# Optimization experiments

Hardware: AMD Instinct MI355X
Metric: run time of the kernel (lower is better)

The kernel has to match this reference:

```python
import jax, jax.numpy as jnp
import numpy as np

NUM_CLASSES = 80
NUM_ANCHORS = 5
ANCHORS = np.array([[1.3221, 1.73145], [3.19275, 4.00944], [5.05587, 8.09892],
                    [9.47112, 4.84053], [11.2364, 10.0071]], dtype=np.float32)
OBJECT_SCALE = 5.0
NOOBJECT_SCALE = 1.0
COORD_SCALE = 1.0
CLASS_SCALE = 1.0
THRESH = 0.6
SEEN = 0  # module initializes self.seen = 0 -> burn-in branch (seen < 12800) active
MAX_BOXES = 50


def _iou_cxcywh(a, b):
    # a, b: (..., 4) center-x, center-y, w, h; broadcastable. Matches multi_bbox_ious(x1y1x2y2=False).
    ax1, ax2 = a[..., 0] - a[..., 2] / 2, a[..., 0] + a[..., 2] / 2
    ay1, ay2 = a[..., 1] - a[..., 3] / 2, a[..., 1] + a[..., 3] / 2
    bx1, bx2 = b[..., 0] - b[..., 2] / 2, b[..., 0] + b[..., 2] / 2
    by1, by2 = b[..., 1] - b[..., 3] / 2, b[..., 1] + b[..., 3] / 2
    iw = jnp.maximum(jnp.minimum(ax2, bx2) - jnp.maximum(ax1, bx1), 0.0)
    ih = jnp.maximum(jnp.minimum(ay2, by2) - jnp.maximum(ay1, by1), 0.0)
    inter = iw * ih
    union = a[..., 2] * a[..., 3] + b[..., 2] * b[..., 3] - inter
    return inter / jnp.maximum(union, 1e-10)


def setup_inputs() -> dict:
    key = jax.random.key(0)
    k1, k2, k3, k4, k5, k6 = jax.random.split(key, 6)
    nB, nH, nW = 64, 38, 38
    output = jax.random.normal(k1, (nB, NUM_ANCHORS * (5 + NUM_CLASSES), nH, nW), dtype=jnp.float32)
    # target rows: (class, x, y, w, h), coords normalized to (0,1); x>0 keeps all 50 boxes valid
    cls = jax.random.randint(k2, (nB, MAX_BOXES), 0, NUM_CLASSES).astype(jnp.float32)
    x = jax.random.uniform(k3, (nB, MAX_BOXES), minval=0.05, maxval=0.95)
    y = jax.random.uniform(k4, (nB, MAX_BOXES), minval=0.05, maxval=0.95)
    w = jax.random.uniform(k5, (nB, MAX_BOXES), minval=0.02, maxval=0.4)
    h = jax.random.uniform(k6, (nB, MAX_BOXES), minval=0.02, maxval=0.4)
    target = jnp.stack([cls, x, y, w, h], axis=-1).reshape(nB, MAX_BOXES * 5)
    return {"output": output, "target": target}


def _forward(output, target):
    nB, nA, nC = output.shape[0], NUM_ANCHORS, NUM_CLASSES
    nH, nW = output.shape[2], output.shape[3]
    N = nB * nA * nH * nW
    anchors = jnp.asarray(ANCHORS)
    f32 = output.dtype

    out5 = output.reshape(nB, nA, 5 + nC, nH, nW)
    txy = jax.nn.sigmoid(out5[:, :, 0:2])  # [nB,nA,2,nH,nW]
    twh = out5[:, :, 2:4]
    conf = jax.nn.sigmoid(out5[:, :, 4]).reshape(N)
    cls_logits = out5[:, :, 5:].transpose(0, 1, 3, 4, 2).reshape(N, nC)
    # coord layout matches torch: [4, nB*nA*nH*nW], rows = (sx, sy, tw, th)
    coord = jnp.concatenate([txy, twh], axis=2).transpose(2, 0, 1, 3, 4).reshape(4, N)

    # decoded pred boxes in grid units; detached like the original (convert2cpu + .detach())
    grid_x = jnp.arange(nW, dtype=f32)
    grid_y = jnp.arange(nH, dtype=f32)[:, None]
    px = txy[:, :, 0] + grid_x
    py = txy[:, :, 1] + grid_y
    pw = jnp.exp(twh[:, :, 0]) * anchors[:, 0][None, :, None, None]
    ph = jnp.exp(twh[:, :, 1]) * anchors[:, 1][None, :, None, None]
    pred_boxes = jax.lax.stop_gradient(jnp.stack([px, py, pw, ph], axis=-1))  # [nB,nA,nH,nW,4]

    # ---------------- build_targets, vectorized over (batch, gt-box) ----------------
    tbox = target.reshape(nB, MAX_BOXES, 5)  # (cls, x, y, w, h)
    # loop breaks at first x == 0 -> prefix-valid mask
    valid = jnp.cumprod((tbox[:, :, 1] > 0).astype(jnp.int32), axis=1).astype(bool)
    gx, gy = tbox[:, :, 1] * nW, tbox[:, :, 2] * nH
    gw, gh = tbox[:, :, 3] * nW, tbox[:, :, 4] * nH
    gt = jnp.stack([gx, gy, gw, gh], axis=-1)  # [nB,50,4]

    # pass 1: ignore mask -- max IoU of every pred box against all valid GTs
    pb_flat = pred_boxes.reshape(nB, nA * nH * nW, 4)
    ious = _iou_cxcywh(pb_flat[:, :, None, :], gt[:, None, :, :])  # [nB,P,50]
    cur_ious = jnp.where(valid[:, None, :], ious, 0.0).max(axis=2)
    noobj = (cur_ious <= THRESH).astype(f32).reshape(N)

    # pass 2: best anchor per GT (both boxes centered at origin -> IoU simplifies)
    aw, ah = anchors[:, 0], anchors[:, 1]
    inter_a = jnp.minimum(aw, gw[..., None]) * jnp.minimum(ah, gh[..., None])  # [nB,50,nA]
    union_a = aw * ah + (gw * gh)[..., None] - inter_a
    best_n = jnp.argmax(inter_a / jnp.maximum(union_a, 1e-10), axis=-1)  # [nB,50]

    gi = jnp.clip(gx.astype(jnp.int32), 0, nW - 1)
    gj = jnp.clip(gy.astype(jnp.int32), 0, nH - 1)
    b_idx = jnp.arange(nB)[:, None]
    pred_sel = pred_boxes[b_idx, best_n, gj, gi]  # [nB,50,4]
    iou_sel = _iou_cxcywh(gt, pred_sel)           # [nB,50]

    fidx = ((b_idx * nA + best_n) * nH + gj) * nW + gi
    fidx = jnp.where(valid, fidx, N)  # invalid boxes -> OOB index, dropped by scatter

    obj = jnp.zeros(N, f32).at[fidx].set(1.0, mode='drop')
    noobj = noobj.at[fidx].set(0.0, mode='drop')
    cm0 = 0.01 if SEEN < 12800 else 0.0
    coord_mask = jnp.full(N, cm0, f32).at[fidx].set(2.0 - tbox[:, :, 3] * tbox[:, :, 4], mode='drop')
    t0 = 0.5 if SEEN < 12800 else 0.0
    tc0 = jnp.full(N, t0, f32).at[fidx].set(gx - gi.astype(f32), mode='drop')
    tc1 = jnp.full(N, t0, f32).at[fidx].set(gy - gj.astype(f32), mode='drop')
    tc2 = jnp.zeros(N, f32).at[fidx].set(jnp.log(gw / aw[best_n]), mode='drop')
    tc3 = jnp.zeros(N, f32).at[fidx].set(jnp.log(gh / ah[best_n]), mode='drop')
    tcoord = jnp.stack([tc0, tc1, tc2, tc3], axis=0)  # [4,N]
    tconf = jnp.zeros(N, f32).at[fidx].set(iou_sel, mode='drop')  # rescore=1
    tcls = jnp.zeros(N, jnp.int32).at[fidx].set(tbox[:, :, 0].astype(jnp.int32), mode='drop')

    # ---------------- losses ----------------
    conf_mask = OBJECT_SCALE * obj + NOOBJECT_SCALE * noobj
    loss_coord = COORD_SCALE * jnp.sum(((coord - tcoord) * coord_mask) ** 2) / nB
    loss_conf = jnp.sum(((conf - tconf) * conf_mask) ** 2) / nB
    logp = jax.nn.log_softmax(cls_logits, axis=-1)
    ce = -jnp.take_along_axis(logp, tcls[:, None], axis=1)[:, 0]  # per-cell CE
    loss_cls = CLASS_SCALE * jnp.sum(obj * ce) / nB  # CE summed only over obj cells
    return loss_coord + loss_conf + loss_cls


def reference(output, target):
    return _forward(output, target)
```

## Files before the change

### kernel.cpp

```cpp
#include <hip/hip_runtime.h>
#include <math.h>

#define NB 64
#define NA 5
#define NC 80
#define NH 38
#define NW 38
#define MAXB 50
#define PLANE (NH*NW)
#define PER_B (NA*PLANE)
#define NCH (5+NC)
#define MAIN_BX ((PER_B + 255) / 256)
#define NPART (MAIN_BX * NB)

__constant__ float c_aw[5] = {1.3221f, 3.19275f, 5.05587f, 9.47112f, 11.2364f};
__constant__ float c_ah[5] = {1.73145f, 4.00944f, 8.09892f, 4.84053f, 10.0071f};

struct Entry {
    int   fidx;
    int   tcls;
    float cm, tc0, tc1, tc2, tc3, tconf;
};

__device__ inline float sigmoidf(float x) { return 1.f / (1.f + expf(-x)); }

__device__ inline float iou_f(float ax, float ay, float aw_, float ah_,
                              float bx, float by, float bw_, float bh_) {
    float ax1 = ax - aw_ * 0.5f, ax2 = ax + aw_ * 0.5f;
    float ay1 = ay - ah_ * 0.5f, ay2 = ay + ah_ * 0.5f;
    float bx1 = bx - bw_ * 0.5f, bx2 = bx + bw_ * 0.5f;
    float by1 = by - bh_ * 0.5f, by2 = by + bh_ * 0.5f;
    float iw = fmaxf(fminf(ax2, bx2) - fmaxf(ax1, bx1), 0.f);
    float ih = fmaxf(fminf(ay2, by2) - fmaxf(ay1, by1), 0.f);
    float inter = iw * ih;
    float uni = aw_ * ah_ + bw_ * bh_ - inter;
    return inter / fmaxf(uni, 1e-10f);
}

__global__ __launch_bounds__(64)
void prep_kernel(const float* __restrict__ out, const float* __restrict__ target,
                 float4* __restrict__ gt, int* __restrict__ nvalid,
                 Entry* __restrict__ entries) {
    int b = blockIdx.x;
    int t = threadIdx.x;
    const float* tb = target + b * MAXB * 5;

    float cls = 0.f, x = 0.f, y = 0.f, w = 0.f, h = 0.f;
    bool has = (t < MAXB);
    if (has) {
        cls = tb[t * 5 + 0];
        x   = tb[t * 5 + 1];
        y   = tb[t * 5 + 2];
        w   = tb[t * 5 + 3];
        h   = tb[t * 5 + 4];
    }
    unsigned long long mask = __ballot(has && (x > 0.f));
    bool valid = has && (((~mask) & ((1ull << (t + 1)) - 1ull)) == 0ull);

    float gx = x * NW, gy = y * NH, gw = w * NW, gh = h * NH;

    int best = 0; float bestr = -1.f;
    #pragma unroll
    for (int a = 0; a < NA; a++) {
        float inter = fminf(c_aw[a], gw) * fminf(c_ah[a], gh);
        float uni   = c_aw[a] * c_ah[a] + gw * gh - inter;
        float r = inter / fmaxf(uni, 1e-10f);
        if (r > bestr) { bestr = r; best = a; }
    }
    int gi = min(max((int)gx, 0), NW - 1);
    int gj = min(max((int)gy, 0), NH - 1);
    int fidx = b * PER_B + best * PLANE + gj * NW + gi;

    float iou_sel = 0.f;
    if (valid) {
        int base = ((b * NA + best) * NCH) * PLANE + gj * NW + gi;
        float o0 = out[base];
        float o1 = out[base + PLANE];
        float o2 = out[base + 2 * PLANE];
        float o3 = out[base + 3 * PLANE];
        float px = sigmoidf(o0) + (float)gi;
        float py = sigmoidf(o1) + (float)gj;
        float pw = expf(o2) * c_aw[best];
        float ph = expf(o3) * c_ah[best];
        iou_sel = iou_f(gx, gy, gw, gh, px, py, pw, ph);
    }

    __shared__ int sfidx[64];
    sfidx[t] = valid ? fidx : -1;
    __syncthreads();
    bool winner = valid;
    if (valid) {
        for (int s = t + 1; s < MAXB; s++) {
            if (sfidx[s] == fidx) { winner = false; break; }
        }
    }

    if (has) {
        gt[b * MAXB + t] = make_float4(gx, gy, gw, gh);
        Entry e;
        e.fidx  = winner ? fidx : -1;
        e.tcls  = (int)cls;
        e.cm    = 2.f - w * h;
        e.tc0   = gx - (float)gi;
        e.tc1   = gy - (float)gj;
        e.tc2   = logf(gw / c_aw[best]);
        e.tc3   = logf(gh / c_ah[best]);
        e.tconf = iou_sel;
        entries[b * MAXB + t] = e;
    }
    if (t == 0) {
        unsigned long long nm = ~mask;
        int cnt = __ffsll((unsigned long long)nm) - 1;
        nvalid[b] = min(cnt, MAXB);
    }
}

__global__ __launch_bounds__(256)
void main_kernel(const float* __restrict__ out,
                 const float4* __restrict__ gt, const int* __restrict__ nvalid,
                 const Entry* __restrict__ entries, float* __restrict__ partial) {
    int b   = blockIdx.y;
    int tid = threadIdx.x;
    int m   = blockIdx.x * blockDim.x + tid;

    __shared__ float4 sgt[MAXB];
    __shared__ Entry  sent[MAXB];
    __shared__ int    snv;
    if (tid < MAXB) {
        sgt[tid]  = gt[b * MAXB + tid];
        sent[tid] = entries[b * MAXB + tid];
    }
    if (tid == 0) snv = nvalid[b];
    __syncthreads();

    float part = 0.f;
    if (m < PER_B) {
        int a   = m / PLANE;
        int pos = m - a * PLANE;
        int j   = pos / NW;
        int i   = pos - j * NW;

        int base = ((b * NA + a) * NCH) * PLANE + pos;
        float o0 = out[base];
        float o1 = out[base + PLANE];
        float o2 = out[base + 2 * PLANE];
        float o3 = out[base + 3 * PLANE];
        float o4 = out[base + 4 * PLANE];

        float s0   = sigmoidf(o0);
        float s1   = sigmoidf(o1);
        float conf = sigmoidf(o4);
        float px = s0 + (float)i;
        float py = s1 + (float)j;
        float pw = expf(o2) * c_aw[a];
        float ph = expf(o3) * c_ah[a];

        float curmax = 0.f;
        int nv = snv;
        for (int s = 0; s < nv; s++) {
            float4 g = sgt[s];
            curmax = fmaxf(curmax, iou_f(px, py, pw, ph, g.x, g.y, g.z, g.w));
        }

        float cm = 0.01f, tc0 = 0.5f, tc1 = 0.5f, tc2 = 0.f, tc3 = 0.f, tconf = 0.f;
        bool is_obj = false;
        int tcls = 0;
        int n = b * PER_B + m;
        for (int s = 0; s < MAXB; s++) {
            if (sent[s].fidx == n) {
                is_obj = true;
                cm  = sent[s].cm;
                tc0 = sent[s].tc0;  tc1 = sent[s].tc1;
                tc2 = sent[s].tc2;  tc3 = sent[s].tc3;
                tconf = sent[s].tconf;
                tcls  = sent[s].tcls;
            }
        }
        float conf_mask = is_obj ? 5.f : ((curmax <= 0.6f) ? 1.f : 0.f);

        float d;
        d = (s0   - tc0)   * cm;        part += d * d;
        d = (s1   - tc1)   * cm;        part += d * d;
        d = (o2   - tc2)   * cm;        part += d * d;
        d = (o3   - tc3)   * cm;        part += d * d;
        d = (conf - tconf) * conf_mask; part += d * d;

        if (is_obj) {
            const float* cp = out + base + 5 * PLANE;
            float mx = -INFINITY, s = 0.f, tv = 0.f;
            for (int c = 0; c < NC; c++) {
                float v = cp[c * PLANE];
                if (c == tcls) tv = v;
                float mn = fmaxf(mx, v);
                s = s * expf(mx - mn) + expf(v - mn);
                mx = mn;
            }
            part += mx + logf(s) - tv;
        }
    }

    for (int off = 32; off > 0; off >>= 1) part += __shfl_down(part, off);
    __shared__ float wsum[4];
    int wid = tid >> 6, lane = tid & 63;
    if (lane == 0) wsum[wid] = part;
    __syncthreads();
    if (tid == 0)
        partial[b * gridDim.x + blockIdx.x] = wsum[0] + wsum[1] + wsum[2] + wsum[3];
}

__global__ __launch_bounds__(256)
void final_kernel(const float* __restrict__ partial, float* __restrict__ loss) {
    int tid = threadIdx.x;
    float s = 0.f;
    for (int i = tid; i < NPART; i += 256) s += partial[i];
    for (int off = 32; off > 0; off >>= 1) s += __shfl_down(s, off);
    __shared__ float wsum[4];
    int wid = tid >> 6, lane = tid & 63;
    if (lane == 0) wsum[wid] = s;
    __syncthreads();
    if (tid == 0)
        loss[0] = (wsum[0] + wsum[1] + wsum[2] + wsum[3]) * (1.0f / NB);
}

extern "C" void kernel_launch(void* const* d_in, const int* in_sizes, int n_in,
                              void* d_out, int out_size, void* d_ws, size_t ws_size,
                              hipStream_t stream) {
    const float* out    = (const float*)d_in[0];
    const float* target = (const float*)d_in[1];
    float* loss = (float*)d_out;

    char* ws = (char*)d_ws;
    float4* gt      = (float4*)ws;
    int*    nvalid  = (int*)(ws + 51200);
    Entry*  entries = (Entry*)(ws + 51456);
    float*  partial = (float*)(ws + 153856);

    prep_kernel<<<NB, 64, 0, stream>>>(out, target, gt, nvalid, entries);

    dim3 grid(MAIN_BX, NB);
    main_kernel<<<grid, 256, 0, stream>>>(out, gt, nvalid, entries, partial);

    final_kernel<<<1, 256, 0, stream>>>(partial, loss);
}
```

Before: 253.5 us.

## Fuse target prep into main loss kernel and precompute GT box corners

```diff
diff --git a/kernel.cpp b/kernel.cpp
--- a/kernel.cpp
+++ b/kernel.cpp
@@ -24,115 +24,109 @@
 
 __device__ inline float sigmoidf(float x) { return 1.f / (1.f + expf(-x)); }
 
-__device__ inline float iou_f(float ax, float ay, float aw_, float ah_,
-                              float bx, float by, float bw_, float bh_) {
-    float ax1 = ax - aw_ * 0.5f, ax2 = ax + aw_ * 0.5f;
-    float ay1 = ay - ah_ * 0.5f, ay2 = ay + ah_ * 0.5f;
-    float bx1 = bx - bw_ * 0.5f, bx2 = bx + bw_ * 0.5f;
-    float by1 = by - bh_ * 0.5f, by2 = by + bh_ * 0.5f;
-    float iw = fmaxf(fminf(ax2, bx2) - fmaxf(ax1, bx1), 0.f);
-    float ih = fmaxf(fminf(ay2, by2) - fmaxf(ay1, by1), 0.f);
-    float inter = iw * ih;
-    float uni = aw_ * ah_ + bw_ * bh_ - inter;
-    return inter / fmaxf(uni, 1e-10f);
-}
-
-__global__ __launch_bounds__(64)
-void prep_kernel(const float* __restrict__ out, const float* __restrict__ target,
-                 float4* __restrict__ gt, int* __restrict__ nvalid,
-                 Entry* __restrict__ entries) {
-    int b = blockIdx.x;
-    int t = threadIdx.x;
-    const float* tb = target + b * MAXB * 5;
-
-    float cls = 0.f, x = 0.f, y = 0.f, w = 0.f, h = 0.f;
-    bool has = (t < MAXB);
-    if (has) {
-        cls = tb[t * 5 + 0];
-        x   = tb[t * 5 + 1];
-        y   = tb[t * 5 + 2];
-        w   = tb[t * 5 + 3];
-        h   = tb[t * 5 + 4];
+__global__ __launch_bounds__(256)
+void main_kernel(const float* __restrict__ out, const float* __restrict__ target,
+                 float* __restrict__ partial) {
+    const int b   = blockIdx.y;
+    const int bx  = blockIdx.x;
+    const int tid = threadIdx.x;
+
+    __shared__ float4 sbox[MAXB];
+    __shared__ float  sarea[MAXB];
+    __shared__ Entry  sent[MAXB];
+    __shared__ int    sfx[64];
+    __shared__ int    snv;
+    __shared__ int    sobj_cnt;
+    __shared__ int    sobj_idx[MAXB];
+
+    if (tid == 0) sobj_cnt = 0;
+
+    if (tid < 64) {
+        const float* tb = target + b * MAXB * 5;
+        int t = tid;
+        bool has = (t < MAXB);
+        float cls = 0.f, x = 0.f, y = 0.f, w = 0.f, h = 0.f;
+        if (has) {
+            cls = tb[t * 5 + 0];
+            x   = tb[t * 5 + 1];
+            y   = tb[t * 5 + 2];
+            w   = tb[t * 5 + 3];
+            h   = tb[t * 5 + 4];
+        }
+        unsigned long long mask = __ballot(has && (x > 0.f));
+        bool valid = has && (((~mask) & ((1ull << (t + 1)) - 1ull)) == 0ull);
+
+        float gx = x * NW, gy = y * NH, gw = w * NW, gh = h * NH;
+
+        int best = 0; float bestr = -1.f;
+        #pragma unroll
+        for (int a = 0; a < NA; a++) {
+            float inter = fminf(c_aw[a], gw) * fminf(c_ah[a], gh);
+            float uni   = c_aw[a] * c_ah[a] + gw * gh - inter;
+            float r = inter / fmaxf(uni, 1e-10f);
+            if (r > bestr) { bestr = r; best = a; }
+        }
+        int gi = min(max((int)gx, 0), NW - 1);
+        int gj = min(max((int)gy, 0), NH - 1);
+        int fidx = b * PER_B + best * PLANE + gj * NW + gi;
+
+        float iou_sel = 0.f;
+        if (valid) {
+            int base = ((b * NA + best) * NCH) * PLANE + gj * NW + gi;
+            float o0 = out[base];
+            float o1 = out[base + PLANE];
+            float o2 = out[base + 2 * PLANE];
+            float o3 = out[base + 3 * PLANE];
+            float px = sigmoidf(o0) + (float)gi;
+            float py = sigmoidf(o1) + (float)gj;
+            float pw = expf(o2) * c_aw[best];
+            float ph = expf(o3) * c_ah[best];
+            float iw = fmaxf(fminf(gx + gw*0.5f, px + pw*0.5f) - fmaxf(gx - gw*0.5f, px - pw*0.5f), 0.f);
+            float ih = fmaxf(fminf(gy + gh*0.5f, py + ph*0.5f) - fmaxf(gy - gh*0.5f, py - ph*0.5f), 0.f);
+            float inter = iw * ih;
+            float uni = gw * gh + pw * ph - inter;
+            iou_sel = inter / fmaxf(uni, 1e-10f);
+        }
+
+        sfx[t] = valid ? fidx : -1;
+        bool winner = valid;
+        if (valid) {
+            for (int s = t + 1; s < MAXB; s++)
+                if (sfx[s] == fidx) { winner = false; break; }
+        }
+
+        if (has) {
+            sbox[t]  = make_float4(gx - gw*0.5f, gy - gh*0.5f, gx + gw*0.5f, gy + gh*0.5f);
+            sarea[t] = gw * gh;
+            Entry e;
+            e.fidx  = winner ? fidx : -1;
+            e.tcls  = (int)cls;
+            e.cm    = 2.f - w * h;
+            e.tc0   = gx - (float)gi;
+            e.tc1   = gy - (float)gj;
+            e.tc2   = logf(gw / c_aw[best]);
+            e.tc3   = logf(gh / c_ah[best]);
+            e.tconf = iou_sel;
+            sent[t] = e;
+        }
+        if (t == 0) {
+            unsigned long long nm = ~mask;
+            snv = min(__ffsll((unsigned long long)nm) - 1, MAXB);
+        }
     }
-    unsigned long long mask = __ballot(has && (x > 0.f));
-    bool valid = has && (((~mask) & ((1ull << (t + 1)) - 1ull)) == 0ull);
-
-    float gx = x * NW, gy = y * NH, gw = w * NW, gh = h * NH;
-
-    int best = 0; float bestr = -1.f;
-    #pragma unroll
-    for (int a = 0; a < NA; a++) {
-        float inter = fminf(c_aw[a], gw) * fminf(c_ah[a], gh);
-        float uni   = c_aw[a] * c_ah[a] + gw * gh - inter;
-        float r = inter / fmaxf(uni, 1e-10f);
-        if (r > bestr) { bestr = r; best = a; }
+    __syncthreads();
+
+    const int nlo = b * PER_B + bx * 256;
+    if (tid < MAXB) {
+        int f = sent[tid].fidx;
+        if (f >= nlo && f < nlo + 256) {
+            int slot = atomicAdd(&sobj_cnt, 1);
+            sobj_idx[slot] = tid;
+        }
     }
-    int gi = min(max((int)gx, 0), NW - 1);
-    int gj = min(max((int)gy, 0), NH - 1);
-    int fidx = b * PER_B + best * PLANE + gj * NW + gi;
-
-    float iou_sel = 0.f;
-    if (valid) {
-        int base = ((b * NA + best) * NCH) * PLANE + gj * NW + gi;
-        float o0 = out[base];
-        float o1 = out[base + PLANE];
-        float o2 = out[base + 2 * PLANE];
-        float o3 = out[base + 3 * PLANE];
-        float px = sigmoidf(o0) + (float)gi;
-        float py = sigmoidf(o1) + (float)gj;
-        float pw = expf(o2) * c_aw[best];
-        float ph = expf(o3) * c_ah[best];
-        iou_sel = iou_f(gx, gy, gw, gh, px, py, pw, ph);
-    }
-
-    __shared__ int sfidx[64];
-    sfidx[t] = valid ? fidx : -1;
-    __syncthreads();
-    bool winner = valid;
-    if (valid) {
-        for (int s = t + 1; s < MAXB; s++) {
-            if (sfidx[s] == fidx) { winner = false; break; }
-        }
-    }
-
-    if (has) {
-        gt[b * MAXB + t] = make_float4(gx, gy, gw, gh);
-        Entry e;
-        e.fidx  = winner ? fidx : -1;
-        e.tcls  = (int)cls;
-        e.cm    = 2.f - w * h;
-        e.tc0   = gx - (float)gi;
-        e.tc1   = gy - (float)gj;
-        e.tc2   = logf(gw / c_aw[best]);
-        e.tc3   = logf(gh / c_ah[best]);
-        e.tconf = iou_sel;
-        entries[b * MAXB + t] = e;
-    }
-    if (t == 0) {
-        unsigned long long nm = ~mask;
-        int cnt = __ffsll((unsigned long long)nm) - 1;
-        nvalid[b] = min(cnt, MAXB);
-    }
-}
-
-__global__ __launch_bounds__(256)
-void main_kernel(const float* __restrict__ out,
-                 const float4* __restrict__ gt, const int* __restrict__ nvalid,
-                 const Entry* __restrict__ entries, float* __restrict__ partial) {
-    int b   = blockIdx.y;
-    int tid = threadIdx.x;
-    int m   = blockIdx.x * blockDim.x + tid;
-
-    __shared__ float4 sgt[MAXB];
-    __shared__ Entry  sent[MAXB];
-    __shared__ int    snv;
-    if (tid < MAXB) {
-        sgt[tid]  = gt[b * MAXB + tid];
-        sent[tid] = entries[b * MAXB + tid];
-    }
-    if (tid == 0) snv = nvalid[b];
-    __syncthreads();
-
+    __syncthreads();
+
+    int m = bx * 256 + tid;
     float part = 0.f;
     if (m < PER_B) {
         int a   = m / PLANE;
@@ -150,33 +144,42 @@
         float s0   = sigmoidf(o0);
         float s1   = sigmoidf(o1);
         float conf = sigmoidf(o4);
-        float px = s0 + (float)i;
-        float py = s1 + (float)j;
         float pw = expf(o2) * c_aw[a];
         float ph = expf(o3) * c_ah[a];
-
-        float curmax = 0.f;
+        float px1 = s0 + (float)i - pw * 0.5f;
+        float px2 = px1 + pw;
+        float py1 = s1 + (float)j - ph * 0.5f;
+        float py2 = py1 + ph;
+        float area_p = pw * ph;
+
+        bool gt06 = false;
         int nv = snv;
         for (int s = 0; s < nv; s++) {
-            float4 g = sgt[s];
-            curmax = fmaxf(curmax, iou_f(px, py, pw, ph, g.x, g.y, g.z, g.w));
+            float4 g = sbox[s];
+            float iw = fmaxf(fminf(px2, g.z) - fmaxf(px1, g.x), 0.f);
+            float ih = fmaxf(fminf(py2, g.w) - fmaxf(py1, g.y), 0.f);
+            float inter = iw * ih;
+            float uni = area_p + sarea[s] - inter;
+            gt06 = gt06 || (inter > 0.6f * fmaxf(uni, 1e-10f));
         }
 
         float cm = 0.01f, tc0 = 0.5f, tc1 = 0.5f, tc2 = 0.f, tc3 = 0.f, tconf = 0.f;
         bool is_obj = false;
         int tcls = 0;
-        int n = b * PER_B + m;
-        for (int s = 0; s < MAXB; s++) {
-            if (sent[s].fidx == n) {
+        int n = nlo + tid;
+        int oc = sobj_cnt;
+        for (int s = 0; s < oc; s++) {
+            int e = sobj_idx[s];
+            if (sent[e].fidx == n) {
                 is_obj = true;
-                cm  = sent[s].cm;
-                tc0 = sent[s].tc0;  tc1 = sent[s].tc1;
-                tc2 = sent[s].tc2;  tc3 = sent[s].tc3;
-                tconf = sent[s].tconf;
-                tcls  = sent[s].tcls;
+                cm  = sent[e].cm;
+                tc0 = sent[e].tc0;  tc1 = sent[e].tc1;
+                tc2 = sent[e].tc2;  tc3 = sent[e].tc3;
+                tconf = sent[e].tconf;
+                tcls  = sent[e].tcls;
             }
         }
-        float conf_mask = is_obj ? 5.f : ((curmax <= 0.6f) ? 1.f : 0.f);
+        float conf_mask = is_obj ? 5.f : (gt06 ? 0.f : 1.f);
 
         float d;
         d = (s0   - tc0)   * cm;        part += d * d;
@@ -205,7 +208,7 @@
     if (lane == 0) wsum[wid] = part;
     __syncthreads();
     if (tid == 0)
-        partial[b * gridDim.x + blockIdx.x] = wsum[0] + wsum[1] + wsum[2] + wsum[3];
+        partial[b * MAIN_BX + bx] = wsum[0] + wsum[1] + wsum[2] + wsum[3];
 }
 
 __global__ __launch_bounds__(256)
@@ -227,18 +230,10 @@
                               hipStream_t stream) {
     const float* out    = (const float*)d_in[0];
     const float* target = (const float*)d_in[1];
-    float* loss = (float*)d_out;
-
-    char* ws = (char*)d_ws;
-    float4* gt      = (float4*)ws;
-    int*    nvalid  = (int*)(ws + 51200);
-    Entry*  entries = (Entry*)(ws + 51456);
-    float*  partial = (float*)(ws + 153856);
-
-    prep_kernel<<<NB, 64, 0, stream>>>(out, target, gt, nvalid, entries);
+    float* loss    = (float*)d_out;
+    float* partial = (float*)d_ws;
 
     dim3 grid(MAIN_BX, NB);
-    main_kernel<<<grid, 256, 0, stream>>>(out, gt, nvalid, entries, partial);
-
+    main_kernel<<<grid, 256, 0, stream>>>(out, target, partial);
     final_kernel<<<1, 256, 0, stream>>>(partial, loss);
 }
```

After: 231.8 us. 1.09x faster.
